# Kernel tuning notes

Hardware: AMD Instinct MI355X
Metric: run time of the kernel (lower is better)

## Reference

```python
import jax, jax.numpy as jnp
import numpy as np

N_NODES = 100000
N_EDGES = 1600000
D = 64  # input_dim = hidden_dim = output_dim
EPS = 1e-12


def _sage_layer(x, src, dst, wl, bl, wr, br):
    # gather messages from source nodes: [E, D]
    msg = x[src]
    # scatter-mean onto destination nodes
    s = jax.ops.segment_sum(msg, dst, num_segments=x.shape[0])
    cnt = jax.ops.segment_sum(jnp.ones((src.shape[0], 1), x.dtype), dst, num_segments=x.shape[0])
    prop = s / jnp.maximum(cnt, 1.0)
    out = x @ wl.T + bl + prop @ wr.T + br
    # F.normalize(out, p=2, dim=1)
    norm = jnp.sqrt(jnp.sum(out * out, axis=1, keepdims=True))
    return out / jnp.maximum(norm, EPS)


def setup_inputs() -> dict:
    key = jax.random.key(0)
    ks = jax.random.split(key, 12)
    d = D

    def lin(k, fan_in, fan_out):
        bound = 1.0 / np.sqrt(fan_in)
        kw, kb = jax.random.split(k)
        w = jax.random.uniform(kw, (fan_out, fan_in), jnp.float32, -bound, bound)
        b = jax.random.uniform(kb, (fan_out,), jnp.float32, -bound, bound)
        return w, b

    x = jax.random.normal(ks[0], (N_NODES, d), jnp.float32)
    edge_index = jax.random.randint(ks[1], (2, N_EDGES), 0, N_NODES, jnp.int64)

    w1l, b1l = lin(ks[2], d, d)
    w1r, b1r = lin(ks[3], d, d)
    w2l, b2l = lin(ks[4], d, d)
    w2r, b2r = lin(ks[5], d, d)
    wp1, bp1 = lin(ks[6], d, d)
    wp2, bp2 = lin(ks[7], d, d)

    return {"x": x, "edge_index": edge_index,
            "w1l": w1l, "b1l": b1l, "w1r": w1r, "b1r": b1r,
            "w2l": w2l, "b2l": b2l, "w2r": w2r, "b2r": b2r,
            "wp1": wp1, "bp1": bp1, "wp2": wp2, "bp2": bp2}


def reference(x, edge_index, w1l, b1l, w1r, b1r, w2l, b2l, w2r, b2r, wp1, bp1, wp2, bp2):
    src = edge_index[0]
    dst = edge_index[1]
    # layer 1: GraphSage -> relu (dropout is identity in eval)
    h = _sage_layer(x, src, dst, w1l, b1l, w1r, b1r)
    h = jax.nn.relu(h)
    # layer 2
    h = _sage_layer(h, src, dst, w2l, b2l, w2r, b2r)
    h = jax.nn.relu(h)
    # post_mp: Linear -> Dropout(identity) -> Linear; emb=True so no log_softmax
    h = h @ wp1.T + bp1
    h = h @ wp2.T + bp2
    return h
```

## Files before the change

### kernel.cpp

```cpp
#include <hip/hip_runtime.h>

#define NN 100000
#define NE 1600000
#define DD 64
#define NB 196
#define BKT 512
#define CAP 9000
#define NOCT 12500
#define NH 391
#define NG1 1024

__launch_bounds__(256)
__global__ void scatter2_kernel(const int* __restrict__ src, const int* __restrict__ dst,
                                int* __restrict__ gcursor, int2* __restrict__ pairs) {
  __shared__ int lh[NB];
  __shared__ int lbase[NB];
  __shared__ int lcur[NB];
  const int NQ = NE / 4;
  int t = blockIdx.x * 256 + threadIdx.x;
  const int nt = NH * 256;
  for (int i = threadIdx.x; i < NB; i += 256) lh[i] = 0;
  __syncthreads();
  int4 dv[4], sv[4];
  bool pv[4];
  #pragma unroll
  for (int k = 0; k < 4; ++k) {
    int idx = t + k * nt;
    pv[k] = idx < NQ;
    if (pv[k]) {
      dv[k] = reinterpret_cast<const int4*>(dst)[idx];
      sv[k] = reinterpret_cast<const int4*>(src)[idx];
      atomicAdd(&lh[dv[k].x >> 9], 1);
      atomicAdd(&lh[dv[k].y >> 9], 1);
      atomicAdd(&lh[dv[k].z >> 9], 1);
      atomicAdd(&lh[dv[k].w >> 9], 1);
    }
  }
  __syncthreads();
  for (int i = threadIdx.x; i < NB; i += 256) {
    lcur[i] = 0;
    lbase[i] = lh[i] ? (i * CAP + atomicAdd(&gcursor[i], lh[i])) : 0;
  }
  __syncthreads();
  #pragma unroll
  for (int k = 0; k < 4; ++k) {
    if (pv[k]) {
      int b;
      b = dv[k].x >> 9; pairs[lbase[b] + atomicAdd(&lcur[b], 1)] = make_int2(sv[k].x, dv[k].x);
      b = dv[k].y >> 9; pairs[lbase[b] + atomicAdd(&lcur[b], 1)] = make_int2(sv[k].y, dv[k].y);
      b = dv[k].z >> 9; pairs[lbase[b] + atomicAdd(&lcur[b], 1)] = make_int2(sv[k].z, dv[k].z);
      b = dv[k].w >> 9; pairs[lbase[b] + atomicAdd(&lcur[b], 1)] = make_int2(sv[k].w, dv[k].w);
    }
  }
}

__launch_bounds__(256)
__global__ void csr_kernel(const int2* __restrict__ pairs, const int* __restrict__ gcursor,
                           int* __restrict__ deg, int* __restrict__ off,
                           int* __restrict__ adj) {
  __shared__ int lh[BKT];
  __shared__ int wsum[4];
  int b = blockIdx.x;
  int t = threadIdx.x;
  int rs = b * CAP, re = rs + gcursor[b];
  lh[2 * t] = 0;
  lh[2 * t + 1] = 0;
  __syncthreads();
  for (int i = rs + t; i < re; i += 256)
    atomicAdd(&lh[pairs[i].y - b * BKT], 1);
  __syncthreads();
  int lane = t & 63, w = t >> 6;
  int h0 = lh[2 * t], h1 = lh[2 * t + 1];
  int s = h0 + h1, incl = s;
  #pragma unroll
  for (int o = 1; o < 64; o <<= 1) {
    int u = __shfl_up(incl, o, 64);
    if (lane >= o) incl += u;
  }
  if (lane == 63) wsum[w] = incl;
  __syncthreads();
  int prefix = 0;
  for (int u = 0; u < w; ++u) prefix += wsum[u];
  int excl = prefix + incl - s;
  int n0 = b * BKT + 2 * t, n1 = n0 + 1;
  if (n0 < NN) { deg[n0] = h0; off[n0] = rs + excl; }
  if (n1 < NN) { deg[n1] = h1; off[n1] = rs + excl + h0; }
  lh[2 * t] = excl;
  lh[2 * t + 1] = excl + h0;
  __syncthreads();
  for (int i = rs + t; i < re; i += 256) {
    int2 e = pairs[i];
    int pos = atomicAdd(&lh[e.y - b * BKT], 1);
    adj[rs + pos] = e.x;
  }
}

__launch_bounds__(256)
__global__ void selfgemm_kernel(const float* __restrict__ x,
                                const float* __restrict__ wl,
                                const float* __restrict__ bl,
                                const float* __restrict__ br,
                                float* __restrict__ tmp,
                                const float* __restrict__ wp1, const float* __restrict__ bp1,
                                const float* __restrict__ wp2, const float* __restrict__ bp2,
                                float* __restrict__ wc4f, float* __restrict__ bc) {
  __shared__ float4 wA4[16 * 64] __attribute__((aligned(16)));
  __shared__ float sp[4][8][DD] __attribute__((aligned(16)));
  int bid = blockIdx.x;
  if (bid < NG1) {
    int tid = threadIdx.x;
    int j = tid & 63;
    int w = tid >> 6;
    float* wAf = (float*)wA4;
    for (int i = tid; i < DD * DD; i += 256) {
      int jj = i >> 6, k = i & 63;
      wAf[(((k >> 2) * 64) + jj) * 4 + (k & 3)] = wl[i];
    }
    float bias = bl[j] + br[j];
    __syncthreads();
    const int ngrp = 3125;
    for (int grp = bid; grp < ngrp; grp += NG1) {
      int n0 = (grp * 4 + w) * 8;
      const float4* xg = reinterpret_cast<const float4*>(&x[(size_t)n0 * DD]);
      float4* spv = reinterpret_cast<float4*>(&sp[w][0][0]);
      spv[j] = xg[j];
      spv[j + 64] = xg[j + 64];
      float acc[8];
      #pragma unroll
      for (int i = 0; i < 8; ++i) acc[i] = bias;
      #pragma unroll
      for (int q = 0; q < 16; ++q) {
        int kb = q * 4;
        float4 wq = wA4[q * 64 + j];
        #pragma unroll
        for (int i = 0; i < 8; ++i) {
          float4 sv = *(const float4*)&sp[w][i][kb];
          float a = acc[i];
          a = fmaf(sv.x, wq.x, a);
          a = fmaf(sv.y, wq.y, a);
          a = fmaf(sv.z, wq.z, a);
          a = fmaf(sv.w, wq.w, a);
          acc[i] = a;
        }
      }
      #pragma unroll
      for (int i = 0; i < 8; ++i) tmp[(size_t)(n0 + i) * DD + j] = acc[i];
    }
  } else {
    int t = threadIdx.x;
    for (int idx = t; idx < DD * DD; idx += 256) {
      int jp = idx >> 6, k = idx & 63;
      float s = 0.f;
      #pragma unroll
      for (int m = 0; m < DD; ++m) s = fmaf(wp2[jp * DD + m], wp1[m * DD + k], s);
      wc4f[(((k >> 2) * 64) + jp) * 4 + (k & 3)] = s;
    }
    if (t < DD) {
      float s = bp2[t];
      #pragma unroll
      for (int m = 0; m < DD; ++m) s = fmaf(wp2[t * DD + m], bp1[m], s);
      bc[t] = s;
    }
  }
}

__launch_bounds__(256)
__global__ void gather_kernel(const float* __restrict__ x,
                              const int* __restrict__ off,
                              const int* __restrict__ deg,
                              const int* __restrict__ adj,
                              float* __restrict__ prop) {
  const float4* X = reinterpret_cast<const float4*>(x);
  int wid = (blockIdx.x * 256 + threadIdx.x) >> 6;
  int nwaves = (gridDim.x * 256) >> 6;
  int lane = threadIdx.x & 63;
  int g = lane >> 4;
  int s = lane & 15;
  const int NQUAD = NN / 4;
  for (int q = wid; q < NQUAD; q += nwaves) {
    int n = q * 4 + g;
    int start = off[n];
    int d = deg[n];
    float4 a0 = {0,0,0,0}, a1 = {0,0,0,0}, a2 = {0,0,0,0}, a3 = {0,0,0,0};
    int t = 0;
    for (; t + 4 <= d; t += 4) {
      int i0 = adj[start + t + 0];
      int i1 = adj[start + t + 1];
      int i2 = adj[start + t + 2];
      int i3 = adj[start + t + 3];
      float4 v0 = X[i0 * 16 + s];
      float4 v1 = X[i1 * 16 + s];
      float4 v2 = X[i2 * 16 + s];
      float4 v3 = X[i3 * 16 + s];
      a0.x += v0.x; a0.y += v0.y; a0.z += v0.z; a0.w += v0.w;
      a1.x += v1.x; a1.y += v1.y; a1.z += v1.z; a1.w += v1.w;
      a2.x += v2.x; a2.y += v2.y; a2.z += v2.z; a2.w += v2.w;
      a3.x += v3.x; a3.y += v3.y; a3.z += v3.z; a3.w += v3.w;
    }
    if (t < d) {
      int dm = d - 1;
      int u1 = (t + 1 < d) ? t + 1 : dm;
      int u2 = (t + 2 < d) ? t + 2 : dm;
      int i0 = adj[start + t];
      int i1 = adj[start + u1];
      int i2 = adj[start + u2];
      float4 v0 = X[i0 * 16 + s];
      float4 v1 = X[i1 * 16 + s];
      float4 v2 = X[i2 * 16 + s];
      a0.x += v0.x; a0.y += v0.y; a0.z += v0.z; a0.w += v0.w;
      if (t + 1 < d) { a1.x += v1.x; a1.y += v1.y; a1.z += v1.z; a1.w += v1.w; }
      if (t + 2 < d) { a2.x += v2.x; a2.y += v2.y; a2.z += v2.z; a2.w += v2.w; }
    }
    float rc = 1.0f / fmaxf((float)d, 1.0f);
    float4 r;
    r.x = ((a0.x + a1.x) + (a2.x + a3.x)) * rc;
    r.y = ((a0.y + a1.y) + (a2.y + a3.y)) * rc;
    r.z = ((a0.z + a1.z) + (a2.z + a3.z)) * rc;
    r.w = ((a0.w + a1.w) + (a2.w + a3.w)) * rc;
    reinterpret_cast<float4*>(prop)[n * 16 + s] = r;
  }
}

__launch_bounds__(512, 4)
__global__ void gemm_light_kernel(float* __restrict__ out,
                                  const float* __restrict__ prop,
                                  const float* __restrict__ wr) {
  __shared__ float4 wrA4[16 * 64] __attribute__((aligned(16)));
  __shared__ float pp[8][8][DD] __attribute__((aligned(16)));
  int tid = threadIdx.x;
  int j = tid & 63;
  int w = tid >> 6;
  float* wrf = (float*)wrA4;
  for (int i = tid; i < DD * DD; i += 512) {
    int jj = i >> 6, k = i & 63;
    wrf[(((k >> 2) * 64) + jj) * 4 + (k & 3)] = wr[i];
  }
  __syncthreads();

  const int ngrp = (NOCT + 7) / 8;
  for (int grp = blockIdx.x; grp < ngrp; grp += gridDim.x) {
    int o = grp * 8 + w;
    if (o >= NOCT) continue;
    int n0 = o * 8;

    const float4* pg = reinterpret_cast<const float4*>(&prop[(size_t)n0 * DD]);
    float4* ppv = reinterpret_cast<float4*>(&pp[w][0][0]);
    ppv[j] = pg[j];
    ppv[j + 64] = pg[j + 64];

    float acc[8];
    #pragma unroll
    for (int i = 0; i < 8; ++i) acc[i] = out[(size_t)(n0 + i) * DD + j];

    #pragma unroll
    for (int q = 0; q < 16; ++q) {
      int kb = q * 4;
      float4 wq = wrA4[q * 64 + j];
      #pragma unroll
      for (int i = 0; i < 8; ++i) {
        float4 pv = *(const float4*)&pp[w][i][kb];
        float a = acc[i];
        a = fmaf(pv.x, wq.x, a);
        a = fmaf(pv.y, wq.y, a);
        a = fmaf(pv.z, wq.z, a);
        a = fmaf(pv.w, wq.w, a);
        acc[i] = a;
      }
    }

    #pragma unroll
    for (int i = 0; i < 8; ++i) {
      float a = acc[i];
      float ss = a * a;
      #pragma unroll
      for (int o2 = 32; o2 > 0; o2 >>= 1) ss += __shfl_xor(ss, o2, 64);
      float ov = a / fmaxf(sqrtf(ss), 1e-12f);
      ov = fmaxf(ov, 0.0f);
      out[(size_t)(n0 + i) * DD + j] = ov;
    }
  }
}

__launch_bounds__(512, 4)
__global__ void sage_post_kernel(const float* __restrict__ xin,
                                 const float* __restrict__ prop,
                                 const float* __restrict__ wl,
                                 const float* __restrict__ bl,
                                 const float* __restrict__ wr,
                                 const float* __restrict__ br,
                                 const float4* __restrict__ wc4,
                                 const float* __restrict__ bc,
                                 float* __restrict__ out) {
  __shared__ float4 wlA4[16 * 64] __attribute__((aligned(16)));
  __shared__ float4 wrA4[16 * 64] __attribute__((aligned(16)));
  __shared__ float sp[8][8][DD] __attribute__((aligned(16)));
  __shared__ float pp[8][8][DD] __attribute__((aligned(16)));
  int tid = threadIdx.x;
  int j = tid & 63;
  int w = tid >> 6;

  float* wlf = (float*)wlA4;
  float* wrf = (float*)wrA4;
  for (int i = tid; i < DD * DD; i += 512) {
    int jj = i >> 6, k = i & 63;
    wlf[(((k >> 2) * 64) + jj) * 4 + (k & 3)] = wl[i];
    wrf[(((k >> 2) * 64) + jj) * 4 + (k & 3)] = wr[i];
  }
  float bias = bl[j] + br[j];
  float bcv = bc[j];
  __syncthreads();

  const int ngrp = (NOCT + 7) / 8;
  for (int grp = blockIdx.x; grp < ngrp; grp += gridDim.x) {
    int o = grp * 8 + w;
    if (o >= NOCT) continue;
    int n0 = o * 8;

    const float4* xg = reinterpret_cast<const float4*>(&xin[(size_t)n0 * DD]);
    const float4* pg = reinterpret_cast<const float4*>(&prop[(size_t)n0 * DD]);
    float4* spv = reinterpret_cast<float4*>(&sp[w][0][0]);
    float4* ppv = reinterpret_cast<float4*>(&pp[w][0][0]);
    spv[j] = xg[j];
    spv[j + 64] = xg[j + 64];
    ppv[j] = pg[j];
    ppv[j + 64] = pg[j + 64];

    float acc[8];
    #pragma unroll
    for (int i = 0; i < 8; ++i) acc[i] = bias;

    #pragma unroll
    for (int q = 0; q < 16; ++q) {
      int kb = q * 4;
      float4 wlq = wlA4[q * 64 + j];
      float4 wrq = wrA4[q * 64 + j];
      #pragma unroll
      for (int i = 0; i < 8; ++i) {
        float4 sv = *(const float4*)&sp[w][i][kb];
        float4 pv = *(const float4*)&pp[w][i][kb];
        float a = acc[i];
        a = fmaf(sv.x, wlq.x, a);
        a = fmaf(sv.y, wlq.y, a);
        a = fmaf(sv.z, wlq.z, a);
        a = fmaf(sv.w, wlq.w, a);
        a = fmaf(pv.x, wrq.x, a);
        a = fmaf(pv.y, wrq.y, a);
        a = fmaf(pv.z, wrq.z, a);
        a = fmaf(pv.w, wrq.w, a);
        acc[i] = a;
      }
    }

    #pragma unroll
    for (int i = 0; i < 8; ++i) {
      float a = acc[i];
      float ss = a * a;
      #pragma unroll
      for (int o2 = 32; o2 > 0; o2 >>= 1) ss += __shfl_xor(ss, o2, 64);
      float ov = a / fmaxf(sqrtf(ss), 1e-12f);
      ov = fmaxf(ov, 0.0f);
      sp[w][i][j] = ov;
    }

    float acc2[8];
    #pragma unroll
    for (int i = 0; i < 8; ++i) acc2[i] = bcv;
    #pragma unroll
    for (int q = 0; q < 16; ++q) {
      int kb = q * 4;
      float4 wq = wc4[q * 64 + j];
      #pragma unroll
      for (int i = 0; i < 8; ++i) {
        float4 hv = *(const float4*)&sp[w][i][kb];
        float a = acc2[i];
        a = fmaf(hv.x, wq.x, a);
        a = fmaf(hv.y, wq.y, a);
        a = fmaf(hv.z, wq.z, a);
        a = fmaf(hv.w, wq.w, a);
        acc2[i] = a;
      }
    }
    #pragma unroll
    for (int i = 0; i < 8; ++i) out[(size_t)(n0 + i) * DD + j] = acc2[i];
  }
}

extern "C" void kernel_launch(void* const* d_in, const int* in_sizes, int n_in,
                              void* d_out, int out_size, void* d_ws, size_t ws_size,
                              hipStream_t stream) {
  const float* x   = (const float*)d_in[0];
  const int*   ei  = (const int*)d_in[1];
  const float* w1l = (const float*)d_in[2];
  const float* b1l = (const float*)d_in[3];
  const float* w1r = (const float*)d_in[4];
  const float* b1r = (const float*)d_in[5];
  const float* w2l = (const float*)d_in[6];
  const float* b2l = (const float*)d_in[7];
  const float* w2r = (const float*)d_in[8];
  const float* b2r = (const float*)d_in[9];
  const float* wp1 = (const float*)d_in[10];
  const float* bp1 = (const float*)d_in[11];
  const float* wp2 = (const float*)d_in[12];
  const float* bp2 = (const float*)d_in[13];
  float* out = (float*)d_out;

  const int* src = ei;
  const int* dst = ei + NE;

  int* deg     = (int*)d_ws;
  int* off     = deg + 102400;
  int* aux     = off + 102400;
  int* gcursor = aux;
  float* wc4f  = (float*)(aux + 1024);
  float* bc    = wc4f + 4096;
  int* adj     = (int*)(bc + 1024);
  float* prop  = (float*)(adj + NB * CAP);
  int2* pairs  = (int2*)prop;

  hipMemsetAsync(gcursor, 0, NB * sizeof(int), stream);
  scatter2_kernel<<<NH, 256, 0, stream>>>(src, dst, gcursor, pairs);
  csr_kernel<<<NB, 256, 0, stream>>>(pairs, gcursor, deg, off, adj);

  selfgemm_kernel<<<NG1 + 1, 256, 0, stream>>>(x, w1l, b1l, b1r, out,
                                               wp1, bp1, wp2, bp2, wc4f, bc);

  gather_kernel<<<2048, 256, 0, stream>>>(x, off, deg, adj, prop);
  gemm_light_kernel<<<1024, 512, 0, stream>>>(out, prop, w1r);

  gather_kernel<<<2048, 256, 0, stream>>>(out, off, deg, adj, prop);
  sage_post_kernel<<<512, 512, 0, stream>>>(out, prop, w2l, b2l, w2r, b2r,
                                            (const float4*)wc4f, bc, out);
}
```

Baseline: 275.4 us.

## Merge edge scatter and self-GEMM into one heterogeneous kernel launch

Combines the edge bucketing scatter kernel and the self-linear GEMM kernel (plus the post-MLP weight precombination) into a single launch, with blocks dispatched by block index into independent roles sharing a union shared-memory buffer. This lets the memory-bound scatter and the compute-heavier GEMM run concurrently and removes one launch plus the serialization gap between them. The shared-memory footprint per block becomes the maximum of both roles, which could reduce occupancy for the scatter blocks.

New measurement: 266.5 us. -3.2%, faster.

```diff
diff --git a/kernel.cpp b/kernel.cpp
--- a/kernel.cpp
+++ b/kernel.cpp
@@ -11,103 +11,63 @@
 #define NG1 1024
 
 __launch_bounds__(256)
-__global__ void scatter2_kernel(const int* __restrict__ src, const int* __restrict__ dst,
-                                int* __restrict__ gcursor, int2* __restrict__ pairs) {
-  __shared__ int lh[NB];
-  __shared__ int lbase[NB];
-  __shared__ int lcur[NB];
-  const int NQ = NE / 4;
-  int t = blockIdx.x * 256 + threadIdx.x;
-  const int nt = NH * 256;
-  for (int i = threadIdx.x; i < NB; i += 256) lh[i] = 0;
-  __syncthreads();
-  int4 dv[4], sv[4];
-  bool pv[4];
-  #pragma unroll
-  for (int k = 0; k < 4; ++k) {
-    int idx = t + k * nt;
-    pv[k] = idx < NQ;
-    if (pv[k]) {
-      dv[k] = reinterpret_cast<const int4*>(dst)[idx];
-      sv[k] = reinterpret_cast<const int4*>(src)[idx];
-      atomicAdd(&lh[dv[k].x >> 9], 1);
-      atomicAdd(&lh[dv[k].y >> 9], 1);
-      atomicAdd(&lh[dv[k].z >> 9], 1);
-      atomicAdd(&lh[dv[k].w >> 9], 1);
-    }
-  }
-  __syncthreads();
-  for (int i = threadIdx.x; i < NB; i += 256) {
-    lcur[i] = 0;
-    lbase[i] = lh[i] ? (i * CAP + atomicAdd(&gcursor[i], lh[i])) : 0;
-  }
-  __syncthreads();
-  #pragma unroll
-  for (int k = 0; k < 4; ++k) {
-    if (pv[k]) {
-      int b;
-      b = dv[k].x >> 9; pairs[lbase[b] + atomicAdd(&lcur[b], 1)] = make_int2(sv[k].x, dv[k].x);
-      b = dv[k].y >> 9; pairs[lbase[b] + atomicAdd(&lcur[b], 1)] = make_int2(sv[k].y, dv[k].y);
-      b = dv[k].z >> 9; pairs[lbase[b] + atomicAdd(&lcur[b], 1)] = make_int2(sv[k].z, dv[k].z);
-      b = dv[k].w >> 9; pairs[lbase[b] + atomicAdd(&lcur[b], 1)] = make_int2(sv[k].w, dv[k].w);
-    }
-  }
-}
-
-__launch_bounds__(256)
-__global__ void csr_kernel(const int2* __restrict__ pairs, const int* __restrict__ gcursor,
-                           int* __restrict__ deg, int* __restrict__ off,
-                           int* __restrict__ adj) {
-  __shared__ int lh[BKT];
-  __shared__ int wsum[4];
-  int b = blockIdx.x;
-  int t = threadIdx.x;
-  int rs = b * CAP, re = rs + gcursor[b];
-  lh[2 * t] = 0;
-  lh[2 * t + 1] = 0;
-  __syncthreads();
-  for (int i = rs + t; i < re; i += 256)
-    atomicAdd(&lh[pairs[i].y - b * BKT], 1);
-  __syncthreads();
-  int lane = t & 63, w = t >> 6;
-  int h0 = lh[2 * t], h1 = lh[2 * t + 1];
-  int s = h0 + h1, incl = s;
-  #pragma unroll
-  for (int o = 1; o < 64; o <<= 1) {
-    int u = __shfl_up(incl, o, 64);
-    if (lane >= o) incl += u;
-  }
-  if (lane == 63) wsum[w] = incl;
-  __syncthreads();
-  int prefix = 0;
-  for (int u = 0; u < w; ++u) prefix += wsum[u];
-  int excl = prefix + incl - s;
-  int n0 = b * BKT + 2 * t, n1 = n0 + 1;
-  if (n0 < NN) { deg[n0] = h0; off[n0] = rs + excl; }
-  if (n1 < NN) { deg[n1] = h1; off[n1] = rs + excl + h0; }
-  lh[2 * t] = excl;
-  lh[2 * t + 1] = excl + h0;
-  __syncthreads();
-  for (int i = rs + t; i < re; i += 256) {
-    int2 e = pairs[i];
-    int pos = atomicAdd(&lh[e.y - b * BKT], 1);
-    adj[rs + pos] = e.x;
-  }
-}
-
-__launch_bounds__(256)
-__global__ void selfgemm_kernel(const float* __restrict__ x,
-                                const float* __restrict__ wl,
-                                const float* __restrict__ bl,
-                                const float* __restrict__ br,
-                                float* __restrict__ tmp,
-                                const float* __restrict__ wp1, const float* __restrict__ bp1,
-                                const float* __restrict__ wp2, const float* __restrict__ bp2,
-                                float* __restrict__ wc4f, float* __restrict__ bc) {
-  __shared__ float4 wA4[16 * 64] __attribute__((aligned(16)));
-  __shared__ float sp[4][8][DD] __attribute__((aligned(16)));
+__global__ void mega_kernel(const int* __restrict__ src, const int* __restrict__ dst,
+                            int* __restrict__ gcursor, int2* __restrict__ pairs,
+                            const float* __restrict__ x,
+                            const float* __restrict__ wl,
+                            const float* __restrict__ bl,
+                            const float* __restrict__ br,
+                            float* __restrict__ tmp,
+                            const float* __restrict__ wp1, const float* __restrict__ bp1,
+                            const float* __restrict__ wp2, const float* __restrict__ bp2,
+                            float* __restrict__ wc4f, float* __restrict__ bc) {
+  __shared__ __attribute__((aligned(16))) char smem[24576];
   int bid = blockIdx.x;
-  if (bid < NG1) {
+
+  if (bid < NH) {
+    int* lh    = (int*)smem;
+    int* lbase = lh + NB;
+    int* lcur  = lbase + NB;
+    const int NQ = NE / 4;
+    int t = bid * 256 + threadIdx.x;
+    const int nt = NH * 256;
+    for (int i = threadIdx.x; i < NB; i += 256) lh[i] = 0;
+    __syncthreads();
+    int4 dv[4], sv[4];
+    bool pv[4];
+    #pragma unroll
+    for (int k = 0; k < 4; ++k) {
+      int idx = t + k * nt;
+      pv[k] = idx < NQ;
+      if (pv[k]) {
+        dv[k] = reinterpret_cast<const int4*>(dst)[idx];
+        sv[k] = reinterpret_cast<const int4*>(src)[idx];
+        atomicAdd(&lh[dv[k].x >> 9], 1);
+        atomicAdd(&lh[dv[k].y >> 9], 1);
+        atomicAdd(&lh[dv[k].z >> 9], 1);
+        atomicAdd(&lh[dv[k].w >> 9], 1);
+      }
+    }
+    __syncthreads();
+    for (int i = threadIdx.x; i < NB; i += 256) {
+      lcur[i] = 0;
+      lbase[i] = lh[i] ? (i * CAP + atomicAdd(&gcursor[i], lh[i])) : 0;
+    }
+    __syncthreads();
+    #pragma unroll
+    for (int k = 0; k < 4; ++k) {
+      if (pv[k]) {
+        int b;
+        b = dv[k].x >> 9; pairs[lbase[b] + atomicAdd(&lcur[b], 1)] = make_int2(sv[k].x, dv[k].x);
+        b = dv[k].y >> 9; pairs[lbase[b] + atomicAdd(&lcur[b], 1)] = make_int2(sv[k].y, dv[k].y);
+        b = dv[k].z >> 9; pairs[lbase[b] + atomicAdd(&lcur[b], 1)] = make_int2(sv[k].z, dv[k].z);
+        b = dv[k].w >> 9; pairs[lbase[b] + atomicAdd(&lcur[b], 1)] = make_int2(sv[k].w, dv[k].w);
+      }
+    }
+  } else if (bid < NH + NG1) {
+    float4* wA4 = (float4*)smem;
+    float (*sp)[8][DD] = (float(*)[8][DD])(smem + 16384);
+    int vb = bid - NH;
     int tid = threadIdx.x;
     int j = tid & 63;
     int w = tid >> 6;
@@ -119,7 +79,7 @@
     float bias = bl[j] + br[j];
     __syncthreads();
     const int ngrp = 3125;
-    for (int grp = bid; grp < ngrp; grp += NG1) {
+    for (int grp = vb; grp < ngrp; grp += NG1) {
       int n0 = (grp * 4 + w) * 8;
       const float4* xg = reinterpret_cast<const float4*>(&x[(size_t)n0 * DD]);
       float4* spv = reinterpret_cast<float4*>(&sp[w][0][0]);
@@ -161,6 +121,47 @@
       for (int m = 0; m < DD; ++m) s = fmaf(wp2[t * DD + m], bp1[m], s);
       bc[t] = s;
     }
+  }
+}
+
+__launch_bounds__(256)
+__global__ void csr_kernel(const int2* __restrict__ pairs, const int* __restrict__ gcursor,
+                           int* __restrict__ deg, int* __restrict__ off,
+                           int* __restrict__ adj) {
+  __shared__ int lh[BKT];
+  __shared__ int wsum[4];
+  int b = blockIdx.x;
+  int t = threadIdx.x;
+  int rs = b * CAP, re = rs + gcursor[b];
+  lh[2 * t] = 0;
+  lh[2 * t + 1] = 0;
+  __syncthreads();
+  for (int i = rs + t; i < re; i += 256)
+    atomicAdd(&lh[pairs[i].y - b * BKT], 1);
+  __syncthreads();
+  int lane = t & 63, w = t >> 6;
+  int h0 = lh[2 * t], h1 = lh[2 * t + 1];
+  int s = h0 + h1, incl = s;
+  #pragma unroll
+  for (int o = 1; o < 64; o <<= 1) {
+    int u = __shfl_up(incl, o, 64);
+    if (lane >= o) incl += u;
+  }
+  if (lane == 63) wsum[w] = incl;
+  __syncthreads();
+  int prefix = 0;
+  for (int u = 0; u < w; ++u) prefix += wsum[u];
+  int excl = prefix + incl - s;
+  int n0 = b * BKT + 2 * t, n1 = n0 + 1;
+  if (n0 < NN) { deg[n0] = h0; off[n0] = rs + excl; }
+  if (n1 < NN) { deg[n1] = h1; off[n1] = rs + excl + h0; }
+  lh[2 * t] = excl;
+  lh[2 * t + 1] = excl + h0;
+  __syncthreads();
+  for (int i = rs + t; i < re; i += 256) {
+    int2 e = pairs[i];
+    int pos = atomicAdd(&lh[e.y - b * BKT], 1);
+    adj[rs + pos] = e.x;
   }
 }
 
@@ -418,11 +419,10 @@
   int2* pairs  = (int2*)prop;
 
   hipMemsetAsync(gcursor, 0, NB * sizeof(int), stream);
-  scatter2_kernel<<<NH, 256, 0, stream>>>(src, dst, gcursor, pairs);
+  mega_kernel<<<NH + NG1 + 1, 256, 0, stream>>>(src, dst, gcursor, pairs,
+                                                x, w1l, b1l, b1r, out,
+                                                wp1, bp1, wp2, bp2, wc4f, bc);
   csr_kernel<<<NB, 256, 0, stream>>>(pairs, gcursor, deg, off, adj);
-
-  selfgemm_kernel<<<NG1 + 1, 256, 0, stream>>>(x, w1l, b1l, b1r, out,
-                                               wp1, bp1, wp2, bp2, wc4f, bc);
 
   gather_kernel<<<2048, 256, 0, stream>>>(x, off, deg, adj, prop);
   gemm_light_kernel<<<1024, 512, 0, stream>>>(out, prop, w1r);
```
